# Optimization experiments

Hardware: AMD Instinct MI355X
Metric: run time of the kernel (lower is better)

The kernel has to match this reference:

```python
import jax, jax.numpy as jnp
import numpy as np

BATCH = 8
HIDDEN = 256          # per-head size == input channels
NUM_HEADS = 9
H_IMG = 48
W_IMG = 48


def make_R(w, h):
    """Relative-position feature tensor R[i,j,k,l] = [dx, dy, dx^2, dy^2, dx*dy]
    with dx = k - i, dy = l - j (matches torch.meshgrid indexing='ij')."""
    gx, gy = jnp.meshgrid(jnp.arange(w), jnp.arange(h), indexing='ij')
    grid = jnp.stack([gx, gy], axis=-1).astype(jnp.float32)        # (w,h,2)
    rel = grid[None, None, :, :, :] - grid[:, :, None, None, :]    # (w,h,w,h,2)
    return jnp.concatenate(
        [rel, rel ** 2, (rel[..., 0] * rel[..., 1])[..., None]], axis=-1
    )                                                              # (w,h,w,h,5)


def setup_inputs() -> dict:
    key = jax.random.key(0)
    k1, k2, k3, k4, k5 = jax.random.split(key, 5)
    hidden_states = jax.random.normal(k1, (BATCH, HIDDEN, H_IMG, W_IMG), dtype=jnp.float32)
    # init per module: centers ~ N(0, init_mu_std=2.0), spreads = 1 + N(0, 0.01)
    attention_centers = 2.0 * jax.random.normal(k2, (NUM_HEADS, 2), dtype=jnp.float32)
    attention_spreads = 1.0 + 0.01 * jax.random.normal(k3, (NUM_HEADS,), dtype=jnp.float32)
    value_w = 0.02 * jax.random.normal(k4, (HIDDEN, NUM_HEADS * HIDDEN), dtype=jnp.float32)
    value_b = 0.02 * jax.random.normal(k5, (HIDDEN,), dtype=jnp.float32)
    return {
        'hidden_states': hidden_states,
        'attention_centers': attention_centers,
        'attention_spreads': attention_spreads,
        'value_w': value_w,
        'value_b': value_b,
    }


def reference(hidden_states, attention_centers, attention_spreads, value_w, value_b):
    b, c, h, w = hidden_states.shape
    x = jnp.transpose(hidden_states, (0, 3, 2, 1))  # (b, w, h, c)

    # heads target vectors (isotropic gaussian): a = c = sigma^2, b = 0
    a = attention_spreads ** 2                       # (H,)
    mu1 = attention_centers[:, 0]
    mu2 = attention_centers[:, 1]
    # t_h = -1/2 * [-2 a mu1, -2 a mu2, a, a, 0] = [a mu1, a mu2, -a/2, -a/2, 0]
    u = jnp.stack([a * mu1, a * mu2, -0.5 * a, -0.5 * a, jnp.zeros_like(a)], axis=-1)  # (H,5)

    R = make_R(w, h)                                               # (w,h,w,h,5)
    scores = jnp.einsum('ijkld,hd->ijhkl', R, u)                   # (w,h,H,w,h)
    probs = jax.nn.softmax(scores.reshape(w, h, NUM_HEADS, -1), axis=-1)
    probs = probs.reshape(w, h, NUM_HEADS, w, h)
    # dropout is identity in eval mode

    vals = jnp.einsum('ijhkl,bkld->bijhd', probs, x)               # (b,w,h,H,c)
    vals = vals.reshape(b, w, h, NUM_HEADS * c)
    out = vals @ value_w.T + value_b                               # (b,w,h,hidden)
    out = jnp.transpose(out, (0, 3, 2, 1))                         # (b,hidden,h,w)
    return out, probs
```

## Files before the change

kernel.cpp:

```cpp
#include <hip/hip_runtime.h>
#include <cstdint>
#include <cstddef>

#define NHEAD 9
#define CHN   256
#define NB    8
#define WH    48
#define SS    2304
#define OUT0  4718592

typedef short bf16x8 __attribute__((ext_vector_type(8)));
typedef float f32x4  __attribute__((ext_vector_type(4)));

__device__ __forceinline__ float bf2f(unsigned int u16) {
    union { unsigned int i; float f; } v; v.i = u16 << 16; return v.f;
}
__device__ __forceinline__ unsigned short f2bf(float f) {
    union { float f; unsigned int i; } v; v.f = f;
    unsigned int x = v.i;
    unsigned int r = x + 0x7fffu + ((x >> 16) & 1u);
    return (unsigned short)(r >> 16);
}

__global__ __launch_bounds__(256) void k_pre(const float* __restrict__ centers,
                                             const float* __restrict__ spreads,
                                             const float* __restrict__ hs,
                                             const float* __restrict__ Wv,
                                             float* __restrict__ p1, float* __restrict__ p2,
                                             unsigned short* __restrict__ p1b,
                                             unsigned short* __restrict__ p2b,
                                             unsigned short* __restrict__ hsb,
                                             unsigned short* __restrict__ WF) {
    int blk = blockIdx.x;
    int t = threadIdx.x;
    if (blk < 108) {
        int lane = t & 63, wave = t >> 6;
        int ridx = blk * 4 + wave;
        int h = ridx / 48, r = ridx % 48;
        float a = spreads[h]; a = a * a;
        float mu1 = centers[2 * h + 0];
        float mu2 = centers[2 * h + 1];
        bool act = lane < 48;
        float dx = (float)(lane - r);
        float q  = -0.5f * a * dx * dx;
        float g1 = act ? (a * mu1 * dx + q) : -INFINITY;
        float g2 = act ? (a * mu2 * dx + q) : -INFINITY;
        float m1 = g1, m2 = g2;
        #pragma unroll
        for (int off = 32; off >= 1; off >>= 1) {
            m1 = fmaxf(m1, __shfl_xor(m1, off));
            m2 = fmaxf(m2, __shfl_xor(m2, off));
        }
        float e1 = act ? expf(g1 - m1) : 0.f;
        float e2 = act ? expf(g2 - m2) : 0.f;
        float s1 = e1, s2 = e2;
        #pragma unroll
        for (int off = 32; off >= 1; off >>= 1) {
            s1 += __shfl_xor(s1, off);
            s2 += __shfl_xor(s2, off);
        }
        float v1 = e1 / s1, v2 = e2 / s2;
        if (act) {
            p1[h * SS + r * 48 + lane] = v1;
            p2[h * SS + r * 48 + lane] = v2;
        }
        p1b[(h * 48 + r) * 64 + lane] = act ? f2bf(v1) : 0;
        p2b[(h * 48 + r) * 64 + lane] = act ? f2bf(v2) : 0;
    } else if (blk < 396) {
        int kb = blk - 108;
        int e  = t;
        const float* src = Wv + (size_t)e * 2304 + kb * 8;
        float4 f0 = *(const float4*)src;
        float4 f1 = *(const float4*)(src + 4);
        uint4 o;
        o.x = (unsigned int)f2bf(f0.x) | ((unsigned int)f2bf(f0.y) << 16);
        o.y = (unsigned int)f2bf(f0.z) | ((unsigned int)f2bf(f0.w) << 16);
        o.z = (unsigned int)f2bf(f1.x) | ((unsigned int)f2bf(f1.y) << 16);
        o.w = (unsigned int)f2bf(f1.z) | ((unsigned int)f2bf(f1.w) << 16);
        *(uint4*)(WF + ((size_t)kb * 256 + e) * 8) = o;
    } else {
        int bd = blk - 396;
        const float* src = hs + (size_t)bd * SS;
        unsigned short* dst = hsb + (size_t)bd * 3072;
        for (int u = t; u < 384; u += 256) {
            int l = u >> 3, c8 = u & 7;
            uint4 o = {0u, 0u, 0u, 0u};
            if (c8 < 6) {
                const float* p = src + l * 48 + c8 * 8;
                float4 f0 = *(const float4*)p;
                float4 f1 = *(const float4*)(p + 4);
                o.x = (unsigned int)f2bf(f0.x) | ((unsigned int)f2bf(f0.y) << 16);
                o.y = (unsigned int)f2bf(f0.z) | ((unsigned int)f2bf(f0.w) << 16);
                o.z = (unsigned int)f2bf(f1.x) | ((unsigned int)f2bf(f1.y) << 16);
                o.w = (unsigned int)f2bf(f1.z) | ((unsigned int)f2bf(f1.w) << 16);
            }
            *(uint4*)(dst + l * 64 + c8 * 8) = o;
        }
    }
}

__global__ __launch_bounds__(256, 2) void k_attn_probs(const unsigned short* __restrict__ hsb,
                                                       const unsigned short* __restrict__ p1b,
                                                       const unsigned short* __restrict__ p2b,
                                                       unsigned short* __restrict__ AF,
                                                       const float* __restrict__ p1,
                                                       const float* __restrict__ p2,
                                                       float* __restrict__ probs,
                                                       int nAttn) {
    int blk = blockIdx.x;
    int t = threadIdx.x;

    if (blk < nAttn) {
        __shared__ unsigned short Sbuf[4 * 3456];
        __shared__ unsigned short Vbuf[8 * 2304];

        int h = blk >> 8;
        int rem = blk & 255;
        int b = rem >> 5, od = rem & 31;
        int d0 = od * 8;
        int kb = h * 32 + od;

        int lane = t & 63, wave = t >> 6;
        int l15 = lane & 15, quad = lane >> 4;

        const bf16x8* P1 = (const bf16x8*)(p1b + (size_t)h * 3072);
        const bf16x8* P2 = (const bf16x8*)(p2b + (size_t)h * 3072);
        bf16x8 pa[3][2], pb[3][2];
        #pragma unroll
        for (int tt = 0; tt < 3; ++tt)
            #pragma unroll
            for (int kt = 0; kt < 2; ++kt) {
                int u = (tt * 16 + l15) * 8 + kt * 4 + quad;
                pa[tt][kt] = P1[u];
                pb[tt][kt] = P2[u];
            }

        unsigned short* Sw = Sbuf + wave * 3456;
        for (int z = lane; z < 384; z += 64) {
            int row = z >> 3;
            *(unsigned int*)(Sw + row * 72 + 48 + ((z & 7) << 1)) = 0u;
        }

        for (int s = 0; s < 2; ++s) {
            int d = d0 + wave * 2 + s;
            int kk = wave * 2 + s;
            size_t bd = (size_t)b * 256 + d;
            const bf16x8* X = (const bf16x8*)(hsb + bd * 3072);

            bf16x8 bx[3][2];
            #pragma unroll
            for (int lt = 0; lt < 3; ++lt)
                #pragma unroll
                for (int kt = 0; kt < 2; ++kt)
                    bx[lt][kt] = X[(lt * 16 + l15) * 8 + kt * 4 + quad];

            f32x4 a1[9];
            #pragma unroll
            for (int q = 0; q < 9; ++q) a1[q] = (f32x4){0.f, 0.f, 0.f, 0.f};
            #pragma unroll
            for (int it = 0; it < 3; ++it)
                #pragma unroll
                for (int lt = 0; lt < 3; ++lt) {
                    a1[it * 3 + lt] = __builtin_amdgcn_mfma_f32_16x16x32_bf16(
                        pa[it][0], bx[lt][0], a1[it * 3 + lt], 0, 0, 0);
                    a1[it * 3 + lt] = __builtin_amdgcn_mfma_f32_16x16x32_bf16(
                        pa[it][1], bx[lt][1], a1[it * 3 + lt], 0, 0, 0);
                }

            #pragma unroll
            for (int it = 0; it < 3; ++it)
                #pragma unroll
                for (int lt = 0; lt < 3; ++lt)
                    #pragma unroll
                    for (int r = 0; r < 4; ++r)
                        Sw[(it * 16 + quad * 4 + r) * 72 + lt * 16 + l15] =
                            f2bf(a1[it * 3 + lt][r]);

            bf16x8 a2f[3][2];
            #pragma unroll
            for (int it = 0; it < 3; ++it)
                #pragma unroll
                for (int kt = 0; kt < 2; ++kt)
                    a2f[it][kt] = *(const bf16x8*)(Sw + (it * 16 + l15) * 72 + kt * 32 + quad * 8);

            f32x4 a2[9];
            #pragma unroll
            for (int q = 0; q < 9; ++q) a2[q] = (f32x4){0.f, 0.f, 0.f, 0.f};
            #pragma unroll
            for (int it = 0; it < 3; ++it)
                #pragma unroll
                for (int jt = 0; jt < 3; ++jt) {
                    a2[it * 3 + jt] = __builtin_amdgcn_mfma_f32_16x16x32_bf16(
                        a2f[it][0], pb[jt][0], a2[it * 3 + jt], 0, 0, 0);
                    a2[it * 3 + jt] = __builtin_amdgcn_mfma_f32_16x16x32_bf16(
                        a2f[it][1], pb[jt][1], a2[it * 3 + jt], 0, 0, 0);
                }

            #pragma unroll
            for (int it = 0; it < 3; ++it)
                #pragma unroll
                for (int jt = 0; jt < 3; ++jt) {
                    f32x4 v = a2[it * 3 + jt];
                    unsigned int lo = (unsigned int)f2bf(v[0]) | ((unsigned int)f2bf(v[1]) << 16);
                    unsigned int hi = (unsigned int)f2bf(v[2]) | ((unsigned int)f2bf(v[3]) << 16);
                    int m = (jt * 16 + l15) * 48 + it * 16 + quad * 4;
                    uint2 u2; u2.x = lo; u2.y = hi;
                    *(uint2*)(Vbuf + kk * 2304 + m) = u2;
                }
        }

        __syncthreads();

        const uint2* Vr = (const uint2*)Vbuf;
        uint4* AFq = (uint4*)AF;
        size_t abase = (size_t)(b * 288 + kb) * 2304;
        for (int g = t; g < 576; g += 256) {
            uint2 rk[8];
            #pragma unroll
            for (int kk = 0; kk < 8; ++kk) rk[kk] = Vr[kk * 576 + g];
            #pragma unroll
            for (int mi = 0; mi < 4; ++mi) {
                unsigned int sel = (mi & 1) ? 0x07060302u : 0x05040100u;
                uint4 o;
                if (mi < 2) {
                    o.x = __builtin_amdgcn_perm(rk[1].x, rk[0].x, sel);
                    o.y = __builtin_amdgcn_perm(rk[3].x, rk[2].x, sel);
                    o.z = __builtin_amdgcn_perm(rk[5].x, rk[4].x, sel);
                    o.w = __builtin_amdgcn_perm(rk[7].x, rk[6].x, sel);
                } else {
                    o.x = __builtin_amdgcn_perm(rk[1].y, rk[0].y, sel);
                    o.y = __builtin_amdgcn_perm(rk[3].y, rk[2].y, sel);
                    o.z = __builtin_amdgcn_perm(rk[5].y, rk[4].y, sel);
                    o.w = __builtin_amdgcn_perm(rk[7].y, rk[6].y, sel);
                }
                AFq[abase + g * 4 + mi] = o;
            }
        }
    } else {
        int pb = blk - nAttn;
        __shared__ float pr1[48];
        __shared__ float4 pr2[12];
        for (int tt = 0; tt < 8; ++tt) {
            int idx = pb * 8 + tt;
            int h = idx % 9; int ij = idx / 9; int j = ij % 48; int i = ij / 48;
            __syncthreads();
            if (t < 48) pr1[t] = p1[(h * 48 + i) * 48 + t];
            else if (t < 60) pr2[t - 48] = ((const float4*)(p2 + (h * 48 + j) * 48))[t - 48];
            __syncthreads();
            f32x4* op = (f32x4*)(probs + (size_t)idx * SS);
            for (int g = t; g < 576; g += 256) {
                int e4 = g * 4;
                int k = e4 / 48, l = e4 % 48;
                float s = pr1[k];
                float4 qv = pr2[l >> 2];
                f32x4 v; v[0] = s * qv.x; v[1] = s * qv.y; v[2] = s * qv.z; v[3] = s * qv.w;
                __builtin_nontemporal_store(v, op + g);
            }
        }
    }
}

__global__ __launch_bounds__(256) void k_gemmC(const unsigned short* __restrict__ AF,
                                               const unsigned short* __restrict__ WF,
                                               const float* __restrict__ vb,
                                               float* __restrict__ out) {
    int blk = blockIdx.x;
    int b = blk / 72; int r = blk % 72; int mb = r >> 1; int nbk = r & 1;
    int t = threadIdx.x;
    int lane = t & 63, wave = t >> 6;
    int l15 = lane & 15, quad = lane >> 4;
    int wm = wave & 1, we = wave >> 1;
    int m0 = mb * 64 + wm * 32;
    int e0 = nbk * 128 + we * 64;

    const bf16x8* pa = (const bf16x8*)AF + (size_t)b * 288 * 2304
                       + (size_t)quad * 2304 + m0 + l15;
    const bf16x8* pw = (const bf16x8*)WF + (size_t)quad * 256 + e0 + l15;

    f32x4 acc[2][4];
    #pragma unroll
    for (int i = 0; i < 2; i++)
        #pragma unroll
        for (int j = 0; j < 4; j++) acc[i][j] = (f32x4){0.f, 0.f, 0.f, 0.f};

    bf16x8 a_cur[2], w_cur[4], a_nxt[2], w_nxt[4];
    a_cur[0] = pa[0];  a_cur[1] = pa[16];
    w_cur[0] = pw[0];  w_cur[1] = pw[16]; w_cur[2] = pw[32]; w_cur[3] = pw[48];

    for (int c = 0; c < 72; ++c) {
        if (c < 71) {
            a_nxt[0] = pa[9216];      a_nxt[1] = pa[9216 + 16];
            w_nxt[0] = pw[1024];      w_nxt[1] = pw[1024 + 16];
            w_nxt[2] = pw[1024 + 32]; w_nxt[3] = pw[1024 + 48];
        }
        #pragma unroll
        for (int tm = 0; tm < 2; ++tm)
            #pragma unroll
            for (int te = 0; te < 4; ++te)
                acc[tm][te] = __builtin_amdgcn_mfma_f32_16x16x32_bf16(
                    a_cur[tm], w_cur[te], acc[tm][te], 0, 0, 0);
        a_cur[0] = a_nxt[0]; a_cur[1] = a_nxt[1];
        w_cur[0] = w_nxt[0]; w_cur[1] = w_nxt[1]; w_cur[2] = w_nxt[2]; w_cur[3] = w_nxt[3];
        pa += 9216; pw += 1024;
    }

    size_t obase = (size_t)b * 589824;
    #pragma unroll
    for (int te = 0; te < 4; ++te) {
        int e = e0 + te * 16 + l15;
        float bias = vb[e];
        #pragma unroll
        for (int tm = 0; tm < 2; ++tm) {
            int m = m0 + tm * 16 + quad * 4;
            float4 v;
            v.x = acc[tm][te][0] + bias;
            v.y = acc[tm][te][1] + bias;
            v.z = acc[tm][te][2] + bias;
            v.w = acc[tm][te][3] + bias;
            *(float4*)(out + obase + (size_t)e * 2304 + m) = v;
        }
    }
}

extern "C" void kernel_launch(void* const* d_in, const int* in_sizes, int n_in,
                              void* d_out, int out_size, void* d_ws, size_t ws_size,
                              hipStream_t stream) {
    const float* hs      = (const float*)d_in[0];
    const float* centers = (const float*)d_in[1];
    const float* spreads = (const float*)d_in[2];
    const float* Wv      = (const float*)d_in[3];
    const float* vbias   = (const float*)d_in[4];

    float* out   = (float*)d_out;
    float* probs = out + OUT0;

    const size_t need = 98973696;
    bool big = ws_size >= need;

    unsigned short *AF, *WF, *hsb, *p1b, *p2b;
    float *p1, *p2;
    if (big) {
        unsigned short* w = (unsigned short*)d_ws;
        AF  = w;
        WF  = AF + 42467328;
        hsb = WF + 589824;
        p1b = hsb + 6291456;
        p2b = p1b + 27648;
        p1  = (float*)(p2b + 27648);
        p2  = p1 + 20736;
    } else {
        p1  = (float*)d_ws;
        p2  = p1 + 20736;
        p1b = (unsigned short*)(p2 + 20736);
        p2b = p1b + 27648;
        AF  = (unsigned short*)probs;
        WF  = AF + 42467328;
        hsb = WF + 589824;
    }

    k_pre<<<2444, 256, 0, stream>>>(centers, spreads, hs, Wv, p1, p2, p1b, p2b, hsb, WF);
    if (big) {
        k_attn_probs<<<2304 + 2592, 256, 0, stream>>>(hsb, p1b, p2b, AF, p1, p2, probs, 2304);
        k_gemmC<<<576, 256, 0, stream>>>(AF, WF, vbias, out);
    } else {
        k_attn_probs<<<2304, 256, 0, stream>>>(hsb, p1b, p2b, AF, p1, p2, probs, 2304);
        k_gemmC<<<576, 256, 0, stream>>>(AF, WF, vbias, out);
        k_attn_probs<<<2592, 256, 0, stream>>>(hsb, p1b, p2b, AF, p1, p2, probs, 0);
    }
}
```

Measured before the change: 327.1 us.

## Fuse all stages into a persistent kernel with global-atomic grid barriers

Replaces the three separate launches (preprocess, attention/probs, output GEMM) with one persistent kernel sized to occupancy. Stages are separated by atomic-counter grid barriers, and probs writing is overlapped with the GEMM tail on idle blocks. The hidden-state bf16 conversion is folded directly into the attention stage, which removes the hsb buffer pass. It also halves the Vbuf shared memory so three blocks fit per CU. The spin barriers depend on all G blocks being co-resident, which the occupancy query is meant to guarantee, and the smaller per-step AF writes are narrower (uint2 instead of uint4).

```diff
diff --git a/kernel.cpp b/kernel.cpp
--- a/kernel.cpp
+++ b/kernel.cpp
@@ -2,19 +2,12 @@
 #include <cstdint>
 #include <cstddef>
 
-#define NHEAD 9
-#define CHN   256
-#define NB    8
-#define WH    48
 #define SS    2304
 #define OUT0  4718592
 
 typedef short bf16x8 __attribute__((ext_vector_type(8)));
 typedef float f32x4  __attribute__((ext_vector_type(4)));
 
-__device__ __forceinline__ float bf2f(unsigned int u16) {
-    union { unsigned int i; float f; } v; v.i = u16 << 16; return v.f;
-}
 __device__ __forceinline__ unsigned short f2bf(float f) {
     union { float f; unsigned int i; } v; v.f = f;
     unsigned int x = v.i;
@@ -22,137 +15,143 @@
     return (unsigned short)(r >> 16);
 }
 
-__global__ __launch_bounds__(256) void k_pre(const float* __restrict__ centers,
-                                             const float* __restrict__ spreads,
-                                             const float* __restrict__ hs,
-                                             const float* __restrict__ Wv,
-                                             float* __restrict__ p1, float* __restrict__ p2,
-                                             unsigned short* __restrict__ p1b,
-                                             unsigned short* __restrict__ p2b,
-                                             unsigned short* __restrict__ hsb,
-                                             unsigned short* __restrict__ WF) {
-    int blk = blockIdx.x;
-    int t = threadIdx.x;
-    if (blk < 108) {
-        int lane = t & 63, wave = t >> 6;
-        int ridx = blk * 4 + wave;
-        int h = ridx / 48, r = ridx % 48;
-        float a = spreads[h]; a = a * a;
-        float mu1 = centers[2 * h + 0];
-        float mu2 = centers[2 * h + 1];
-        bool act = lane < 48;
-        float dx = (float)(lane - r);
-        float q  = -0.5f * a * dx * dx;
-        float g1 = act ? (a * mu1 * dx + q) : -INFINITY;
-        float g2 = act ? (a * mu2 * dx + q) : -INFINITY;
-        float m1 = g1, m2 = g2;
-        #pragma unroll
-        for (int off = 32; off >= 1; off >>= 1) {
-            m1 = fmaxf(m1, __shfl_xor(m1, off));
-            m2 = fmaxf(m2, __shfl_xor(m2, off));
-        }
-        float e1 = act ? expf(g1 - m1) : 0.f;
-        float e2 = act ? expf(g2 - m2) : 0.f;
-        float s1 = e1, s2 = e2;
-        #pragma unroll
-        for (int off = 32; off >= 1; off >>= 1) {
-            s1 += __shfl_xor(s1, off);
-            s2 += __shfl_xor(s2, off);
-        }
-        float v1 = e1 / s1, v2 = e2 / s2;
-        if (act) {
-            p1[h * SS + r * 48 + lane] = v1;
-            p2[h * SS + r * 48 + lane] = v2;
-        }
-        p1b[(h * 48 + r) * 64 + lane] = act ? f2bf(v1) : 0;
-        p2b[(h * 48 + r) * 64 + lane] = act ? f2bf(v2) : 0;
-    } else if (blk < 396) {
-        int kb = blk - 108;
-        int e  = t;
-        const float* src = Wv + (size_t)e * 2304 + kb * 8;
-        float4 f0 = *(const float4*)src;
-        float4 f1 = *(const float4*)(src + 4);
-        uint4 o;
-        o.x = (unsigned int)f2bf(f0.x) | ((unsigned int)f2bf(f0.y) << 16);
-        o.y = (unsigned int)f2bf(f0.z) | ((unsigned int)f2bf(f0.w) << 16);
-        o.z = (unsigned int)f2bf(f1.x) | ((unsigned int)f2bf(f1.y) << 16);
-        o.w = (unsigned int)f2bf(f1.z) | ((unsigned int)f2bf(f1.w) << 16);
-        *(uint4*)(WF + ((size_t)kb * 256 + e) * 8) = o;
-    } else {
-        int bd = blk - 396;
-        const float* src = hs + (size_t)bd * SS;
-        unsigned short* dst = hsb + (size_t)bd * 3072;
-        for (int u = t; u < 384; u += 256) {
-            int l = u >> 3, c8 = u & 7;
-            uint4 o = {0u, 0u, 0u, 0u};
-            if (c8 < 6) {
-                const float* p = src + l * 48 + c8 * 8;
-                float4 f0 = *(const float4*)p;
-                float4 f1 = *(const float4*)(p + 4);
-                o.x = (unsigned int)f2bf(f0.x) | ((unsigned int)f2bf(f0.y) << 16);
-                o.y = (unsigned int)f2bf(f0.z) | ((unsigned int)f2bf(f0.w) << 16);
-                o.z = (unsigned int)f2bf(f1.x) | ((unsigned int)f2bf(f1.y) << 16);
-                o.w = (unsigned int)f2bf(f1.z) | ((unsigned int)f2bf(f1.w) << 16);
-            }
-            *(uint4*)(dst + l * 64 + c8 * 8) = o;
-        }
-    }
-}
-
-__global__ __launch_bounds__(256, 2) void k_attn_probs(const unsigned short* __restrict__ hsb,
-                                                       const unsigned short* __restrict__ p1b,
-                                                       const unsigned short* __restrict__ p2b,
-                                                       unsigned short* __restrict__ AF,
-                                                       const float* __restrict__ p1,
-                                                       const float* __restrict__ p2,
-                                                       float* __restrict__ probs,
-                                                       int nAttn) {
-    int blk = blockIdx.x;
-    int t = threadIdx.x;
-
-    if (blk < nAttn) {
-        __shared__ unsigned short Sbuf[4 * 3456];
-        __shared__ unsigned short Vbuf[8 * 2304];
-
-        int h = blk >> 8;
-        int rem = blk & 255;
+__device__ __forceinline__ void probs_unit(int u, int t,
+                                           const float* __restrict__ p1,
+                                           const float* __restrict__ p2,
+                                           float* __restrict__ probs) {
+    #pragma unroll 2
+    for (int tt = 0; tt < 8; ++tt) {
+        int idx = u * 8 + tt;
+        int h = idx % 9; int ij = idx / 9; int j = ij % 48; int i = ij / 48;
+        const float* r1 = p1 + (h * 48 + i) * 48;
+        const float4* r2 = (const float4*)(p2 + (h * 48 + j) * 48);
+        f32x4* op = (f32x4*)(probs + (size_t)idx * SS);
+        for (int g = t; g < 576; g += 256) {
+            int k = g / 12, lq = g % 12;
+            float s = r1[k];
+            float4 q = r2[lq];
+            f32x4 v; v[0] = s * q.x; v[1] = s * q.y; v[2] = s * q.z; v[3] = s * q.w;
+            __builtin_nontemporal_store(v, op + g);
+        }
+    }
+}
+
+__global__ __launch_bounds__(256, 3) void k_mega(
+        const float* __restrict__ hs, const float* __restrict__ centers,
+        const float* __restrict__ spreads, const float* __restrict__ Wv,
+        const float* __restrict__ vb,
+        float* __restrict__ out, float* __restrict__ probs,
+        unsigned short* __restrict__ AF, unsigned short* __restrict__ WF,
+        unsigned short* __restrict__ p1b, unsigned short* __restrict__ p2b,
+        float* __restrict__ p1, float* __restrict__ p2,
+        unsigned* __restrict__ cnt, int G, int writeProbs) {
+    __shared__ unsigned short Sbuf[4 * 3456];
+    __shared__ unsigned short Vbuf[4 * 2304];
+
+    int bl = blockIdx.x, t = threadIdx.x;
+    int lane = t & 63, wave = t >> 6;
+    int l15 = lane & 15, quad = lane >> 4;
+
+    for (int u = bl; u < 396; u += G) {
+        if (u < 108) {
+            int ridx = u * 4 + wave;
+            int h = ridx / 48, r = ridx % 48;
+            float a = spreads[h]; a = a * a;
+            float mu1 = centers[2 * h + 0];
+            float mu2 = centers[2 * h + 1];
+            bool act = lane < 48;
+            float dx = (float)(lane - r);
+            float q  = -0.5f * a * dx * dx;
+            float g1 = act ? (a * mu1 * dx + q) : -INFINITY;
+            float g2 = act ? (a * mu2 * dx + q) : -INFINITY;
+            float m1 = g1, m2 = g2;
+            #pragma unroll
+            for (int off = 32; off >= 1; off >>= 1) {
+                m1 = fmaxf(m1, __shfl_xor(m1, off));
+                m2 = fmaxf(m2, __shfl_xor(m2, off));
+            }
+            float e1 = act ? expf(g1 - m1) : 0.f;
+            float e2 = act ? expf(g2 - m2) : 0.f;
+            float s1 = e1, s2 = e2;
+            #pragma unroll
+            for (int off = 32; off >= 1; off >>= 1) {
+                s1 += __shfl_xor(s1, off);
+                s2 += __shfl_xor(s2, off);
+            }
+            float v1 = e1 / s1, v2 = e2 / s2;
+            if (act) {
+                p1[h * SS + r * 48 + lane] = v1;
+                p2[h * SS + r * 48 + lane] = v2;
+            }
+            p1b[(h * 48 + r) * 64 + lane] = act ? f2bf(v1) : 0;
+            p2b[(h * 48 + r) * 64 + lane] = act ? f2bf(v2) : 0;
+        } else {
+            int kb = u - 108;
+            const float* src = Wv + (size_t)t * 2304 + kb * 8;
+            float4 f0 = *(const float4*)src;
+            float4 f1 = *(const float4*)(src + 4);
+            uint4 o;
+            o.x = (unsigned int)f2bf(f0.x) | ((unsigned int)f2bf(f0.y) << 16);
+            o.y = (unsigned int)f2bf(f0.z) | ((unsigned int)f2bf(f0.w) << 16);
+            o.z = (unsigned int)f2bf(f1.x) | ((unsigned int)f2bf(f1.y) << 16);
+            o.w = (unsigned int)f2bf(f1.z) | ((unsigned int)f2bf(f1.w) << 16);
+            *(uint4*)(WF + ((size_t)kb * 256 + t) * 8) = o;
+        }
+    }
+
+    __threadfence();
+    __syncthreads();
+    if (t == 0) {
+        __hip_atomic_fetch_add(cnt, 1u, __ATOMIC_ACQ_REL, __HIP_MEMORY_SCOPE_AGENT);
+        while (__hip_atomic_load(cnt, __ATOMIC_ACQUIRE, __HIP_MEMORY_SCOPE_AGENT) < (unsigned)G)
+            __builtin_amdgcn_s_sleep(8);
+    }
+    __syncthreads();
+    __threadfence();
+
+    for (int u = bl; u < 2304; u += G) {
+        int h = u >> 8;
+        int rem = u & 255;
         int b = rem >> 5, od = rem & 31;
         int d0 = od * 8;
         int kb = h * 32 + od;
 
-        int lane = t & 63, wave = t >> 6;
-        int l15 = lane & 15, quad = lane >> 4;
-
-        const bf16x8* P1 = (const bf16x8*)(p1b + (size_t)h * 3072);
-        const bf16x8* P2 = (const bf16x8*)(p2b + (size_t)h * 3072);
+        const bf16x8* P1f = (const bf16x8*)(p1b + (size_t)h * 3072);
+        const bf16x8* P2f = (const bf16x8*)(p2b + (size_t)h * 3072);
         bf16x8 pa[3][2], pb[3][2];
         #pragma unroll
         for (int tt = 0; tt < 3; ++tt)
             #pragma unroll
             for (int kt = 0; kt < 2; ++kt) {
-                int u = (tt * 16 + l15) * 8 + kt * 4 + quad;
-                pa[tt][kt] = P1[u];
-                pb[tt][kt] = P2[u];
+                int ui = (tt * 16 + l15) * 8 + kt * 4 + quad;
+                pa[tt][kt] = P1f[ui];
+                pb[tt][kt] = P2f[ui];
             }
 
         unsigned short* Sw = Sbuf + wave * 3456;
-        for (int z = lane; z < 384; z += 64) {
-            int row = z >> 3;
-            *(unsigned int*)(Sw + row * 72 + 48 + ((z & 7) << 1)) = 0u;
-        }
 
         for (int s = 0; s < 2; ++s) {
-            int d = d0 + wave * 2 + s;
-            int kk = wave * 2 + s;
+            int d = d0 + s * 4 + wave;
             size_t bd = (size_t)b * 256 + d;
-            const bf16x8* X = (const bf16x8*)(hsb + bd * 3072);
+            const float* X = hs + bd * SS;
 
             bf16x8 bx[3][2];
             #pragma unroll
             for (int lt = 0; lt < 3; ++lt)
                 #pragma unroll
-                for (int kt = 0; kt < 2; ++kt)
-                    bx[lt][kt] = X[(lt * 16 + l15) * 8 + kt * 4 + quad];
+                for (int kt = 0; kt < 2; ++kt) {
+                    bf16x8 r = {0, 0, 0, 0, 0, 0, 0, 0};
+                    if (kt == 0 || quad < 2) {
+                        const float* px = X + (lt * 16 + l15) * 48 + kt * 32 + quad * 8;
+                        float4 f0 = *(const float4*)px;
+                        float4 f1 = *(const float4*)(px + 4);
+                        r[0] = (short)f2bf(f0.x); r[1] = (short)f2bf(f0.y);
+                        r[2] = (short)f2bf(f0.z); r[3] = (short)f2bf(f0.w);
+                        r[4] = (short)f2bf(f1.x); r[5] = (short)f2bf(f1.y);
+                        r[6] = (short)f2bf(f1.z); r[7] = (short)f2bf(f1.w);
+                    }
+                    bx[lt][kt] = r;
+                }
 
             f32x4 a1[9];
             #pragma unroll
@@ -178,10 +177,13 @@
 
             bf16x8 a2f[3][2];
             #pragma unroll
-            for (int it = 0; it < 3; ++it)
-                #pragma unroll
-                for (int kt = 0; kt < 2; ++kt)
-                    a2f[it][kt] = *(const bf16x8*)(Sw + (it * 16 + l15) * 72 + kt * 32 + quad * 8);
+            for (int it = 0; it < 3; ++it) {
+                a2f[it][0] = *(const bf16x8*)(Sw + (it * 16 + l15) * 72 + quad * 8);
+                if (quad < 2)
+                    a2f[it][1] = *(const bf16x8*)(Sw + (it * 16 + l15) * 72 + 32 + quad * 8);
+                else
+                    a2f[it][1] = (bf16x8){0, 0, 0, 0, 0, 0, 0, 0};
+            }
 
             f32x4 a2[9];
             #pragma unroll
@@ -205,121 +207,121 @@
                     unsigned int hi = (unsigned int)f2bf(v[2]) | ((unsigned int)f2bf(v[3]) << 16);
                     int m = (jt * 16 + l15) * 48 + it * 16 + quad * 4;
                     uint2 u2; u2.x = lo; u2.y = hi;
-                    *(uint2*)(Vbuf + kk * 2304 + m) = u2;
-                }
-        }
-
+                    *(uint2*)(Vbuf + wave * 2304 + m) = u2;
+                }
+
+            __syncthreads();
+            {
+                const uint2* Vr = (const uint2*)Vbuf;
+                unsigned short* AFbase = AF + ((size_t)(b * 288 + kb) * 2304) * 8 + s * 4;
+                for (int g = t; g < 576; g += 256) {
+                    uint2 rk[4];
+                    #pragma unroll
+                    for (int kk = 0; kk < 4; ++kk) rk[kk] = Vr[kk * 576 + g];
+                    #pragma unroll
+                    for (int mi = 0; mi < 4; ++mi) {
+                        unsigned int sel = (mi & 1) ? 0x07060302u : 0x05040100u;
+                        unsigned int s01, s23;
+                        if (mi < 2) {
+                            s01 = __builtin_amdgcn_perm(rk[1].x, rk[0].x, sel);
+                            s23 = __builtin_amdgcn_perm(rk[3].x, rk[2].x, sel);
+                        } else {
+                            s01 = __builtin_amdgcn_perm(rk[1].y, rk[0].y, sel);
+                            s23 = __builtin_amdgcn_perm(rk[3].y, rk[2].y, sel);
+                        }
+                        uint2 o; o.x = s01; o.y = s23;
+                        *(uint2*)(AFbase + (size_t)(4 * g + mi) * 8) = o;
+                    }
+                }
+            }
+            __syncthreads();
+        }
+    }
+
+    __threadfence();
+    __syncthreads();
+    if (t == 0)
+        __hip_atomic_fetch_add(cnt + 1, 1u, __ATOMIC_ACQ_REL, __HIP_MEMORY_SCOPE_AGENT);
+
+    if (writeProbs) {
+        int idleBlocks = G - 576;
+        int PA = (idleBlocks > 0) ? 1536 : 2592;
+        for (int u = bl; u < PA; u += G) probs_unit(u, t, p1, p2, probs);
+        if (idleBlocks > 0 && bl >= 576)
+            for (int u = 1536 + (bl - 576); u < 2592; u += idleBlocks)
+                probs_unit(u, t, p1, p2, probs);
+    }
+
+    if (bl < 576) {
+        if (t == 0) {
+            while (__hip_atomic_load(cnt + 1, __ATOMIC_ACQUIRE, __HIP_MEMORY_SCOPE_AGENT) < (unsigned)G)
+                __builtin_amdgcn_s_sleep(8);
+        }
         __syncthreads();
-
-        const uint2* Vr = (const uint2*)Vbuf;
-        uint4* AFq = (uint4*)AF;
-        size_t abase = (size_t)(b * 288 + kb) * 2304;
-        for (int g = t; g < 576; g += 256) {
-            uint2 rk[8];
-            #pragma unroll
-            for (int kk = 0; kk < 8; ++kk) rk[kk] = Vr[kk * 576 + g];
-            #pragma unroll
-            for (int mi = 0; mi < 4; ++mi) {
-                unsigned int sel = (mi & 1) ? 0x07060302u : 0x05040100u;
-                uint4 o;
-                if (mi < 2) {
-                    o.x = __builtin_amdgcn_perm(rk[1].x, rk[0].x, sel);
-                    o.y = __builtin_amdgcn_perm(rk[3].x, rk[2].x, sel);
-                    o.z = __builtin_amdgcn_perm(rk[5].x, rk[4].x, sel);
-                    o.w = __builtin_amdgcn_perm(rk[7].x, rk[6].x, sel);
-                } else {
-                    o.x = __builtin_amdgcn_perm(rk[1].y, rk[0].y, sel);
-                    o.y = __builtin_amdgcn_perm(rk[3].y, rk[2].y, sel);
-                    o.z = __builtin_amdgcn_perm(rk[5].y, rk[4].y, sel);
-                    o.w = __builtin_amdgcn_perm(rk[7].y, rk[6].y, sel);
-                }
-                AFq[abase + g * 4 + mi] = o;
-            }
-        }
-    } else {
-        int pb = blk - nAttn;
-        __shared__ float pr1[48];
-        __shared__ float4 pr2[12];
-        for (int tt = 0; tt < 8; ++tt) {
-            int idx = pb * 8 + tt;
-            int h = idx % 9; int ij = idx / 9; int j = ij % 48; int i = ij / 48;
-            __syncthreads();
-            if (t < 48) pr1[t] = p1[(h * 48 + i) * 48 + t];
-            else if (t < 60) pr2[t - 48] = ((const float4*)(p2 + (h * 48 + j) * 48))[t - 48];
-            __syncthreads();
-            f32x4* op = (f32x4*)(probs + (size_t)idx * SS);
-            for (int g = t; g < 576; g += 256) {
-                int e4 = g * 4;
-                int k = e4 / 48, l = e4 % 48;
-                float s = pr1[k];
-                float4 qv = pr2[l >> 2];
-                f32x4 v; v[0] = s * qv.x; v[1] = s * qv.y; v[2] = s * qv.z; v[3] = s * qv.w;
-                __builtin_nontemporal_store(v, op + g);
-            }
-        }
-    }
-}
-
-__global__ __launch_bounds__(256) void k_gemmC(const unsigned short* __restrict__ AF,
-                                               const unsigned short* __restrict__ WF,
-                                               const float* __restrict__ vb,
-                                               float* __restrict__ out) {
-    int blk = blockIdx.x;
-    int b = blk / 72; int r = blk % 72; int mb = r >> 1; int nbk = r & 1;
-    int t = threadIdx.x;
-    int lane = t & 63, wave = t >> 6;
-    int l15 = lane & 15, quad = lane >> 4;
-    int wm = wave & 1, we = wave >> 1;
-    int m0 = mb * 64 + wm * 32;
-    int e0 = nbk * 128 + we * 64;
-
-    const bf16x8* pa = (const bf16x8*)AF + (size_t)b * 288 * 2304
-                       + (size_t)quad * 2304 + m0 + l15;
-    const bf16x8* pw = (const bf16x8*)WF + (size_t)quad * 256 + e0 + l15;
-
-    f32x4 acc[2][4];
-    #pragma unroll
-    for (int i = 0; i < 2; i++)
-        #pragma unroll
-        for (int j = 0; j < 4; j++) acc[i][j] = (f32x4){0.f, 0.f, 0.f, 0.f};
-
-    bf16x8 a_cur[2], w_cur[4], a_nxt[2], w_nxt[4];
-    a_cur[0] = pa[0];  a_cur[1] = pa[16];
-    w_cur[0] = pw[0];  w_cur[1] = pw[16]; w_cur[2] = pw[32]; w_cur[3] = pw[48];
-
-    for (int c = 0; c < 72; ++c) {
-        if (c < 71) {
-            a_nxt[0] = pa[9216];      a_nxt[1] = pa[9216 + 16];
-            w_nxt[0] = pw[1024];      w_nxt[1] = pw[1024 + 16];
-            w_nxt[2] = pw[1024 + 32]; w_nxt[3] = pw[1024 + 48];
-        }
-        #pragma unroll
-        for (int tm = 0; tm < 2; ++tm)
-            #pragma unroll
-            for (int te = 0; te < 4; ++te)
-                acc[tm][te] = __builtin_amdgcn_mfma_f32_16x16x32_bf16(
-                    a_cur[tm], w_cur[te], acc[tm][te], 0, 0, 0);
-        a_cur[0] = a_nxt[0]; a_cur[1] = a_nxt[1];
-        w_cur[0] = w_nxt[0]; w_cur[1] = w_nxt[1]; w_cur[2] = w_nxt[2]; w_cur[3] = w_nxt[3];
-        pa += 9216; pw += 1024;
-    }
-
-    size_t obase = (size_t)b * 589824;
-    #pragma unroll
-    for (int te = 0; te < 4; ++te) {
-        int e = e0 + te * 16 + l15;
-        float bias = vb[e];
-        #pragma unroll
-        for (int tm = 0; tm < 2; ++tm) {
-            int m = m0 + tm * 16 + quad * 4;
-            float4 v;
-            v.x = acc[tm][te][0] + bias;
-            v.y = acc[tm][te][1] + bias;
-            v.z = acc[tm][te][2] + bias;
-            v.w = acc[tm][te][3] + bias;
-            *(float4*)(out + obase + (size_t)e * 2304 + m) = v;
-        }
-    }
+        __threadfence();
+
+        for (int u = bl; u < 576; u += G) {
+            int b = u / 72; int r = u % 72; int mb = r >> 1; int nbk = r & 1;
+            int wm = wave & 1, we = wave >> 1;
+            int m0 = mb * 64 + wm * 32;
+            int e0 = nbk * 128 + we * 64;
+
+            const bf16x8* pA = (const bf16x8*)AF + (size_t)b * 288 * 2304
+                               + (size_t)quad * 2304 + m0 + l15;
+            const bf16x8* pW = (const bf16x8*)WF + (size_t)quad * 256 + e0 + l15;
+
+            f32x4 acc[2][4];
+            #pragma unroll
+            for (int i = 0; i < 2; i++)
+                #pragma unroll
+                for (int j = 0; j < 4; j++) acc[i][j] = (f32x4){0.f, 0.f, 0.f, 0.f};
+
+            bf16x8 a_cur[2], w_cur[4], a_nxt[2], w_nxt[4];
+            a_cur[0] = pA[0];  a_cur[1] = pA[16];
+            w_cur[0] = pW[0];  w_cur[1] = pW[16]; w_cur[2] = pW[32]; w_cur[3] = pW[48];
+
+            for (int c = 0; c < 72; ++c) {
+                if (c < 71) {
+                    a_nxt[0] = pA[9216];      a_nxt[1] = pA[9216 + 16];
+                    w_nxt[0] = pW[1024];      w_nxt[1] = pW[1024 + 16];
+                    w_nxt[2] = pW[1024 + 32]; w_nxt[3] = pW[1024 + 48];
+                }
+                #pragma unroll
+                for (int tm = 0; tm < 2; ++tm)
+                    #pragma unroll
+                    for (int te = 0; te < 4; ++te)
+                        acc[tm][te] = __builtin_amdgcn_mfma_f32_16x16x32_bf16(
+                            a_cur[tm], w_cur[te], acc[tm][te], 0, 0, 0);
+                a_cur[0] = a_nxt[0]; a_cur[1] = a_nxt[1];
+                w_cur[0] = w_nxt[0]; w_cur[1] = w_nxt[1];
+                w_cur[2] = w_nxt[2]; w_cur[3] = w_nxt[3];
+                pA += 9216; pW += 1024;
+            }
+
+            size_t obase = (size_t)b * 589824;
+            #pragma unroll
+            for (int te = 0; te < 4; ++te) {
+                int e = e0 + te * 16 + l15;
+                float bias = vb[e];
+                #pragma unroll
+                for (int tm = 0; tm < 2; ++tm) {
+                    int m = m0 + tm * 16 + quad * 4;
+                    float4 v;
+                    v.x = acc[tm][te][0] + bias;
+                    v.y = acc[tm][te][1] + bias;
+                    v.z = acc[tm][te][2] + bias;
+                    v.w = acc[tm][te][3] + bias;
+                    *(float4*)(out + obase + (size_t)e * SS + m) = v;
+                }
+            }
+        }
+    }
+}
+
+__global__ __launch_bounds__(256) void k_probs_sep(const float* __restrict__ p1,
+                                                   const float* __restrict__ p2,
+                                                   float* __restrict__ probs) {
+    probs_unit(blockIdx.x, threadIdx.x, p1, p2, probs);
 }
 
 extern "C" void kernel_launch(void* const* d_in, const int* in_sizes, int n_in,
@@ -334,37 +336,43 @@
     float* out   = (float*)d_out;
     float* probs = out + OUT0;
 
-    const size_t need = 98973696;
-    bool big = ws_size >= need;
-
-    unsigned short *AF, *WF, *hsb, *p1b, *p2b;
+    int occ = 0;
+    if (hipOccupancyMaxActiveBlocksPerMultiprocessor(&occ, k_mega, 256, 0) != hipSuccess || occ <= 0)
+        occ = 2;
+    int G = occ * 256; if (G > 768) G = 768;
+
+    const size_t needBig = 86224896ull + 165888ull + 256ull;
+    bool big = ws_size >= needBig;
+
+    unsigned short *AF, *WF, *p1b, *p2b;
     float *p1, *p2;
+    unsigned* cnt;
     if (big) {
         unsigned short* w = (unsigned short*)d_ws;
         AF  = w;
         WF  = AF + 42467328;
-        hsb = WF + 589824;
-        p1b = hsb + 6291456;
+        p1b = WF + 589824;
         p2b = p1b + 27648;
         p1  = (float*)(p2b + 27648);
         p2  = p1 + 20736;
+        cnt = (unsigned*)(p2 + 20736);
     } else {
-        p1  = (float*)d_ws;
+        cnt = (unsigned*)d_ws;
+        p1  = (float*)((char*)d_ws + 256);
         p2  = p1 + 20736;
         p1b = (unsigned short*)(p2 + 20736);
         p2b = p1b + 27648;
         AF  = (unsigned short*)probs;
         WF  = AF + 42467328;
-        hsb = WF + 589824;
-    }
-
-    k_pre<<<2444, 256, 0, stream>>>(centers, spreads, hs, Wv, p1, p2, p1b, p2b, hsb, WF);
+    }
+
+    hipMemsetAsync(cnt, 0, 64, stream);
     if (big) {
-        k_attn_probs<<<2304 + 2592, 256, 0, stream>>>(hsb, p1b, p2b, AF, p1, p2, probs, 2304);
-        k_gemmC<<<576, 256, 0, stream>>>(AF, WF, vbias, out);
+        k_mega<<<G, 256, 0, stream>>>(hs, centers, spreads, Wv, vbias, out, probs,
+                                      AF, WF, p1b, p2b, p1, p2, cnt, G, 1);
     } else {
-        k_attn_probs<<<2304, 256, 0, stream>>>(hsb, p1b, p2b, AF, p1, p2, probs, 2304);
-        k_gemmC<<<576, 256, 0, stream>>>(AF, WF, vbias, out);
-        k_attn_probs<<<2592, 256, 0, stream>>>(hsb, p1b, p2b, AF, p1, p2, probs, 0);
-    }
-}
+        k_mega<<<G, 256, 0, stream>>>(hs, centers, spreads, Wv, vbias, out, probs,
+                                      AF, WF, p1b, p2b, p1, p2, cnt, G, 0);
+        k_probs_sep<<<2592, 256, 0, stream>>>(p1, p2, probs);
+    }
+}
```

Result: slower. 559.4 us (+71.0%).

## Split attention kernel, fuse probs writing into GEMM tail, reuse shared buffer

Applied to the files above, without the earlier changes.

The probs-only blocks move out of the attention kernel and into the GEMM kernel's grid, so the large probs store overlaps the value-projection GEMM rather than the attention MFMA work. The attention kernel drops to a single shared buffer, reused for the Vbuf transpose with an extra barrier, and raises launch bounds to 3 blocks per CU. The GEMM block shape changes from 64x128 to 32x256 per block. Probs generation now reads p1/p2 straight from global memory instead of staging them through shared memory. The risks are extra register pressure from holding both s-iteration accumulators and changed GEMM tile efficiency.

```diff
diff --git a/kernel.cpp b/kernel.cpp
--- a/kernel.cpp
+++ b/kernel.cpp
@@ -2,19 +2,12 @@
 #include <cstdint>
 #include <cstddef>
 
-#define NHEAD 9
-#define CHN   256
-#define NB    8
-#define WH    48
 #define SS    2304
 #define OUT0  4718592
 
 typedef short bf16x8 __attribute__((ext_vector_type(8)));
 typedef float f32x4  __attribute__((ext_vector_type(4)));
 
-__device__ __forceinline__ float bf2f(unsigned int u16) {
-    union { unsigned int i; float f; } v; v.i = u16 << 16; return v.f;
-}
 __device__ __forceinline__ unsigned short f2bf(float f) {
     union { float f; unsigned int i; } v; v.f = f;
     unsigned int x = v.i;
@@ -99,179 +92,184 @@
     }
 }
 
-__global__ __launch_bounds__(256, 2) void k_attn_probs(const unsigned short* __restrict__ hsb,
-                                                       const unsigned short* __restrict__ p1b,
-                                                       const unsigned short* __restrict__ p2b,
-                                                       unsigned short* __restrict__ AF,
-                                                       const float* __restrict__ p1,
-                                                       const float* __restrict__ p2,
-                                                       float* __restrict__ probs,
-                                                       int nAttn) {
+__global__ __launch_bounds__(256, 3) void k_attn(const unsigned short* __restrict__ hsb,
+                                                 const unsigned short* __restrict__ p1b,
+                                                 const unsigned short* __restrict__ p2b,
+                                                 unsigned short* __restrict__ AF) {
+    __shared__ unsigned short LSH[18432];
+
     int blk = blockIdx.x;
-    int t = threadIdx.x;
-
-    if (blk < nAttn) {
-        __shared__ unsigned short Sbuf[4 * 3456];
-        __shared__ unsigned short Vbuf[8 * 2304];
-
-        int h = blk >> 8;
-        int rem = blk & 255;
-        int b = rem >> 5, od = rem & 31;
-        int d0 = od * 8;
-        int kb = h * 32 + od;
-
-        int lane = t & 63, wave = t >> 6;
-        int l15 = lane & 15, quad = lane >> 4;
-
-        const bf16x8* P1 = (const bf16x8*)(p1b + (size_t)h * 3072);
-        const bf16x8* P2 = (const bf16x8*)(p2b + (size_t)h * 3072);
-        bf16x8 pa[3][2], pb[3][2];
-        #pragma unroll
-        for (int tt = 0; tt < 3; ++tt)
-            #pragma unroll
-            for (int kt = 0; kt < 2; ++kt) {
-                int u = (tt * 16 + l15) * 8 + kt * 4 + quad;
-                pa[tt][kt] = P1[u];
-                pb[tt][kt] = P2[u];
-            }
-
-        unsigned short* Sw = Sbuf + wave * 3456;
-        for (int z = lane; z < 384; z += 64) {
-            int row = z >> 3;
-            *(unsigned int*)(Sw + row * 72 + 48 + ((z & 7) << 1)) = 0u;
-        }
-
-        for (int s = 0; s < 2; ++s) {
-            int d = d0 + wave * 2 + s;
-            int kk = wave * 2 + s;
-            size_t bd = (size_t)b * 256 + d;
-            const bf16x8* X = (const bf16x8*)(hsb + bd * 3072);
-
-            bf16x8 bx[3][2];
-            #pragma unroll
-            for (int lt = 0; lt < 3; ++lt)
-                #pragma unroll
-                for (int kt = 0; kt < 2; ++kt)
-                    bx[lt][kt] = X[(lt * 16 + l15) * 8 + kt * 4 + quad];
-
-            f32x4 a1[9];
-            #pragma unroll
-            for (int q = 0; q < 9; ++q) a1[q] = (f32x4){0.f, 0.f, 0.f, 0.f};
-            #pragma unroll
-            for (int it = 0; it < 3; ++it)
-                #pragma unroll
-                for (int lt = 0; lt < 3; ++lt) {
-                    a1[it * 3 + lt] = __builtin_amdgcn_mfma_f32_16x16x32_bf16(
-                        pa[it][0], bx[lt][0], a1[it * 3 + lt], 0, 0, 0);
-                    a1[it * 3 + lt] = __builtin_amdgcn_mfma_f32_16x16x32_bf16(
-                        pa[it][1], bx[lt][1], a1[it * 3 + lt], 0, 0, 0);
-                }
-
-            #pragma unroll
-            for (int it = 0; it < 3; ++it)
-                #pragma unroll
-                for (int lt = 0; lt < 3; ++lt)
-                    #pragma unroll
-                    for (int r = 0; r < 4; ++r)
-                        Sw[(it * 16 + quad * 4 + r) * 72 + lt * 16 + l15] =
-                            f2bf(a1[it * 3 + lt][r]);
-
-            bf16x8 a2f[3][2];
-            #pragma unroll
-            for (int it = 0; it < 3; ++it)
-                #pragma unroll
-                for (int kt = 0; kt < 2; ++kt)
-                    a2f[it][kt] = *(const bf16x8*)(Sw + (it * 16 + l15) * 72 + kt * 32 + quad * 8);
-
-            f32x4 a2[9];
-            #pragma unroll
-            for (int q = 0; q < 9; ++q) a2[q] = (f32x4){0.f, 0.f, 0.f, 0.f};
-            #pragma unroll
-            for (int it = 0; it < 3; ++it)
-                #pragma unroll
-                for (int jt = 0; jt < 3; ++jt) {
-                    a2[it * 3 + jt] = __builtin_amdgcn_mfma_f32_16x16x32_bf16(
-                        a2f[it][0], pb[jt][0], a2[it * 3 + jt], 0, 0, 0);
-                    a2[it * 3 + jt] = __builtin_amdgcn_mfma_f32_16x16x32_bf16(
-                        a2f[it][1], pb[jt][1], a2[it * 3 + jt], 0, 0, 0);
-                }
-
-            #pragma unroll
-            for (int it = 0; it < 3; ++it)
-                #pragma unroll
-                for (int jt = 0; jt < 3; ++jt) {
-                    f32x4 v = a2[it * 3 + jt];
-                    unsigned int lo = (unsigned int)f2bf(v[0]) | ((unsigned int)f2bf(v[1]) << 16);
-                    unsigned int hi = (unsigned int)f2bf(v[2]) | ((unsigned int)f2bf(v[3]) << 16);
-                    int m = (jt * 16 + l15) * 48 + it * 16 + quad * 4;
-                    uint2 u2; u2.x = lo; u2.y = hi;
-                    *(uint2*)(Vbuf + kk * 2304 + m) = u2;
-                }
-        }
-
-        __syncthreads();
-
-        const uint2* Vr = (const uint2*)Vbuf;
-        uint4* AFq = (uint4*)AF;
-        size_t abase = (size_t)(b * 288 + kb) * 2304;
-        for (int g = t; g < 576; g += 256) {
-            uint2 rk[8];
-            #pragma unroll
-            for (int kk = 0; kk < 8; ++kk) rk[kk] = Vr[kk * 576 + g];
-            #pragma unroll
-            for (int mi = 0; mi < 4; ++mi) {
-                unsigned int sel = (mi & 1) ? 0x07060302u : 0x05040100u;
-                uint4 o;
-                if (mi < 2) {
-                    o.x = __builtin_amdgcn_perm(rk[1].x, rk[0].x, sel);
-                    o.y = __builtin_amdgcn_perm(rk[3].x, rk[2].x, sel);
-                    o.z = __builtin_amdgcn_perm(rk[5].x, rk[4].x, sel);
-                    o.w = __builtin_amdgcn_perm(rk[7].x, rk[6].x, sel);
-                } else {
-                    o.x = __builtin_amdgcn_perm(rk[1].y, rk[0].y, sel);
-                    o.y = __builtin_amdgcn_perm(rk[3].y, rk[2].y, sel);
-                    o.z = __builtin_amdgcn_perm(rk[5].y, rk[4].y, sel);
-                    o.w = __builtin_amdgcn_perm(rk[7].y, rk[6].y, sel);
-                }
-                AFq[abase + g * 4 + mi] = o;
-            }
-        }
-    } else {
-        int pb = blk - nAttn;
-        __shared__ float pr1[48];
-        __shared__ float4 pr2[12];
-        for (int tt = 0; tt < 8; ++tt) {
-            int idx = pb * 8 + tt;
-            int h = idx % 9; int ij = idx / 9; int j = ij % 48; int i = ij / 48;
-            __syncthreads();
-            if (t < 48) pr1[t] = p1[(h * 48 + i) * 48 + t];
-            else if (t < 60) pr2[t - 48] = ((const float4*)(p2 + (h * 48 + j) * 48))[t - 48];
-            __syncthreads();
-            f32x4* op = (f32x4*)(probs + (size_t)idx * SS);
-            for (int g = t; g < 576; g += 256) {
-                int e4 = g * 4;
-                int k = e4 / 48, l = e4 % 48;
-                float s = pr1[k];
-                float4 qv = pr2[l >> 2];
-                f32x4 v; v[0] = s * qv.x; v[1] = s * qv.y; v[2] = s * qv.z; v[3] = s * qv.w;
-                __builtin_nontemporal_store(v, op + g);
-            }
-        }
-    }
-}
-
-__global__ __launch_bounds__(256) void k_gemmC(const unsigned short* __restrict__ AF,
-                                               const unsigned short* __restrict__ WF,
-                                               const float* __restrict__ vb,
-                                               float* __restrict__ out) {
-    int blk = blockIdx.x;
-    int b = blk / 72; int r = blk % 72; int mb = r >> 1; int nbk = r & 1;
+    int h = blk >> 8;
+    int rem = blk & 255;
+    int b = rem >> 5, od = rem & 31;
+    int d0 = od * 8;
+    int kb = h * 32 + od;
+
     int t = threadIdx.x;
     int lane = t & 63, wave = t >> 6;
     int l15 = lane & 15, quad = lane >> 4;
-    int wm = wave & 1, we = wave >> 1;
-    int m0 = mb * 64 + wm * 32;
-    int e0 = nbk * 128 + we * 64;
+
+    const bf16x8* P1 = (const bf16x8*)(p1b + (size_t)h * 3072);
+    const bf16x8* P2 = (const bf16x8*)(p2b + (size_t)h * 3072);
+    bf16x8 pa[3][2], pb[3][2];
+    #pragma unroll
+    for (int tt = 0; tt < 3; ++tt)
+        #pragma unroll
+        for (int kt = 0; kt < 2; ++kt) {
+            int u = (tt * 16 + l15) * 8 + kt * 4 + quad;
+            pa[tt][kt] = P1[u];
+            pb[tt][kt] = P2[u];
+        }
+
+    unsigned short* Sw = LSH + wave * 3456;
+    for (int z = lane; z < 384; z += 64) {
+        int row = z >> 3;
+        *(unsigned int*)(Sw + row * 72 + 48 + ((z & 7) << 1)) = 0u;
+    }
+
+    f32x4 a2k[2][9];
+
+    #pragma unroll
+    for (int s = 0; s < 2; ++s) {
+        int d = d0 + wave * 2 + s;
+        size_t bd = (size_t)b * 256 + d;
+        const bf16x8* X = (const bf16x8*)(hsb + bd * 3072);
+
+        bf16x8 bx[3][2];
+        #pragma unroll
+        for (int lt = 0; lt < 3; ++lt)
+            #pragma unroll
+            for (int kt = 0; kt < 2; ++kt)
+                bx[lt][kt] = X[(lt * 16 + l15) * 8 + kt * 4 + quad];
+
+        f32x4 a1[9];
+        #pragma unroll
+        for (int q = 0; q < 9; ++q) a1[q] = (f32x4){0.f, 0.f, 0.f, 0.f};
+        #pragma unroll
+        for (int it = 0; it < 3; ++it)
+            #pragma unroll
+            for (int lt = 0; lt < 3; ++lt) {
+                a1[it * 3 + lt] = __builtin_amdgcn_mfma_f32_16x16x32_bf16(
+                    pa[it][0], bx[lt][0], a1[it * 3 + lt], 0, 0, 0);
+                a1[it * 3 + lt] = __builtin_amdgcn_mfma_f32_16x16x32_bf16(
+                    pa[it][1], bx[lt][1], a1[it * 3 + lt], 0, 0, 0);
+            }
+
+        #pragma unroll
+        for (int it = 0; it < 3; ++it)
+            #pragma unroll
+            for (int lt = 0; lt < 3; ++lt)
+                #pragma unroll
+                for (int r = 0; r < 4; ++r)
+                    Sw[(it * 16 + quad * 4 + r) * 72 + lt * 16 + l15] =
+                        f2bf(a1[it * 3 + lt][r]);
+
+        bf16x8 a2f[3][2];
+        #pragma unroll
+        for (int it = 0; it < 3; ++it)
+            #pragma unroll
+            for (int kt = 0; kt < 2; ++kt)
+                a2f[it][kt] = *(const bf16x8*)(Sw + (it * 16 + l15) * 72 + kt * 32 + quad * 8);
+
+        #pragma unroll
+        for (int q = 0; q < 9; ++q) a2k[s][q] = (f32x4){0.f, 0.f, 0.f, 0.f};
+        #pragma unroll
+        for (int it = 0; it < 3; ++it)
+            #pragma unroll
+            for (int jt = 0; jt < 3; ++jt) {
+                a2k[s][it * 3 + jt] = __builtin_amdgcn_mfma_f32_16x16x32_bf16(
+                    a2f[it][0], pb[jt][0], a2k[s][it * 3 + jt], 0, 0, 0);
+                a2k[s][it * 3 + jt] = __builtin_amdgcn_mfma_f32_16x16x32_bf16(
+                    a2f[it][1], pb[jt][1], a2k[s][it * 3 + jt], 0, 0, 0);
+            }
+    }
+
+    __syncthreads();
+    #pragma unroll
+    for (int s = 0; s < 2; ++s) {
+        int kk = wave * 2 + s;
+        #pragma unroll
+        for (int it = 0; it < 3; ++it)
+            #pragma unroll
+            for (int jt = 0; jt < 3; ++jt) {
+                f32x4 v = a2k[s][it * 3 + jt];
+                unsigned int lo = (unsigned int)f2bf(v[0]) | ((unsigned int)f2bf(v[1]) << 16);
+                unsigned int hi = (unsigned int)f2bf(v[2]) | ((unsigned int)f2bf(v[3]) << 16);
+                int m = (jt * 16 + l15) * 48 + it * 16 + quad * 4;
+                uint2 u2; u2.x = lo; u2.y = hi;
+                *(uint2*)(LSH + kk * 2304 + m) = u2;
+            }
+    }
+    __syncthreads();
+
+    const uint2* Vr = (const uint2*)LSH;
+    uint4* AFq = (uint4*)AF;
+    size_t abase = (size_t)(b * 288 + kb) * 2304;
+    for (int g = t; g < 576; g += 256) {
+        uint2 rk[8];
+        #pragma unroll
+        for (int kk = 0; kk < 8; ++kk) rk[kk] = Vr[kk * 576 + g];
+        #pragma unroll
+        for (int mi = 0; mi < 4; ++mi) {
+            unsigned int sel = (mi & 1) ? 0x07060302u : 0x05040100u;
+            uint4 o;
+            if (mi < 2) {
+                o.x = __builtin_amdgcn_perm(rk[1].x, rk[0].x, sel);
+                o.y = __builtin_amdgcn_perm(rk[3].x, rk[2].x, sel);
+                o.z = __builtin_amdgcn_perm(rk[5].x, rk[4].x, sel);
+                o.w = __builtin_amdgcn_perm(rk[7].x, rk[6].x, sel);
+            } else {
+                o.x = __builtin_amdgcn_perm(rk[1].y, rk[0].y, sel);
+                o.y = __builtin_amdgcn_perm(rk[3].y, rk[2].y, sel);
+                o.z = __builtin_amdgcn_perm(rk[5].y, rk[4].y, sel);
+                o.w = __builtin_amdgcn_perm(rk[7].y, rk[6].y, sel);
+            }
+            AFq[abase + g * 4 + mi] = o;
+        }
+    }
+}
+
+__device__ __forceinline__ void probs_unit(int u, int t,
+                                           const float* __restrict__ p1,
+                                           const float* __restrict__ p2,
+                                           float* __restrict__ probs) {
+    #pragma unroll 2
+    for (int tt = 0; tt < 8; ++tt) {
+        int idx = u * 8 + tt;
+        int h = idx % 9; int ij = idx / 9; int j = ij % 48; int i = ij / 48;
+        const float* r1 = p1 + (h * 48 + i) * 48;
+        const float4* r2 = (const float4*)(p2 + (h * 48 + j) * 48);
+        f32x4* op = (f32x4*)(probs + (size_t)idx * SS);
+        for (int g = t; g < 576; g += 256) {
+            int k = g / 12, lq = g % 12;
+            float s = r1[k];
+            float4 q = r2[lq];
+            f32x4 v; v[0] = s * q.x; v[1] = s * q.y; v[2] = s * q.z; v[3] = s * q.w;
+            __builtin_nontemporal_store(v, op + g);
+        }
+    }
+}
+
+__global__ __launch_bounds__(256) void k_tail(const unsigned short* __restrict__ AF,
+                                              const unsigned short* __restrict__ WF,
+                                              const float* __restrict__ vb,
+                                              float* __restrict__ out,
+                                              const float* __restrict__ p1,
+                                              const float* __restrict__ p2,
+                                              float* __restrict__ probs) {
+    int blk = blockIdx.x;
+    int t = threadIdx.x;
+
+    if (blk >= 576) {
+        probs_unit(blk - 576, t, p1, p2, probs);
+        return;
+    }
+
+    int b = blk / 72, mb = blk % 72;
+    int lane = t & 63, wave = t >> 6;
+    int l15 = lane & 15, quad = lane >> 4;
+    int m0 = mb * 32;
+    int e0 = wave * 64;
 
     const bf16x8* pa = (const bf16x8*)AF + (size_t)b * 288 * 2304
                        + (size_t)quad * 2304 + m0 + l15;
@@ -317,9 +315,15 @@
             v.y = acc[tm][te][1] + bias;
             v.z = acc[tm][te][2] + bias;
             v.w = acc[tm][te][3] + bias;
-            *(float4*)(out + obase + (size_t)e * 2304 + m) = v;
-        }
-    }
+            *(float4*)(out + obase + (size_t)e * SS + m) = v;
+        }
+    }
+}
+
+__global__ __launch_bounds__(256) void k_probs_sep(const float* __restrict__ p1,
+                                                   const float* __restrict__ p2,
+                                                   float* __restrict__ probs) {
+    probs_unit(blockIdx.x, threadIdx.x, p1, p2, probs);
 }
 
 extern "C" void kernel_launch(void* const* d_in, const int* in_sizes, int n_in,
@@ -334,8 +338,8 @@
     float* out   = (float*)d_out;
     float* probs = out + OUT0;
 
-    const size_t need = 98973696;
-    bool big = ws_size >= need;
+    const size_t needBig = 99000000;
+    bool big = ws_size >= needBig;
 
     unsigned short *AF, *WF, *hsb, *p1b, *p2b;
     float *p1, *p2;
@@ -359,12 +363,11 @@
     }
 
     k_pre<<<2444, 256, 0, stream>>>(centers, spreads, hs, Wv, p1, p2, p1b, p2b, hsb, WF);
+    k_attn<<<2304, 256, 0, stream>>>(hsb, p1b, p2b, AF);
     if (big) {
-        k_attn_probs<<<2304 + 2592, 256, 0, stream>>>(hsb, p1b, p2b, AF, p1, p2, probs, 2304);
-        k_gemmC<<<576, 256, 0, stream>>>(AF, WF, vbias, out);
+        k_tail<<<576 + 2592, 256, 0, stream>>>(AF, WF, vbias, out, p1, p2, probs);
     } else {
-        k_attn_probs<<<2304, 256, 0, stream>>>(hsb, p1b, p2b, AF, p1, p2, probs, 2304);
-        k_gemmC<<<576, 256, 0, stream>>>(AF, WF, vbias, out);
-        k_attn_probs<<<2592, 256, 0, stream>>>(hsb, p1b, p2b, AF, p1, p2, probs, 0);
-    }
-}
+        k_tail<<<576, 256, 0, stream>>>(AF, WF, vbias, out, p1, p2, probs);
+        k_probs_sep<<<2592, 256, 0, stream>>>(p1, p2, probs);
+    }
+}
```

Measured after the change: 305.0 us. -6.7%, faster.
